# Kernel tuning notes

Hardware: AMD Instinct MI355X
Metric: run time of the kernel (lower is better)

## Reference

```python
import jax, jax.numpy as jnp
import numpy as np

GROUPS = 32
EPS = 1e-6


def group_norm(x, gamma, beta):
    b, c, h, w = x.shape
    xg = x.reshape(b, GROUPS, c // GROUPS, h, w)
    mean = xg.mean(axis=(2, 3, 4), keepdims=True)
    var = xg.var(axis=(2, 3, 4), keepdims=True)
    xn = (xg - mean) * jax.lax.rsqrt(var + EPS)
    xn = xn.reshape(b, c, h, w)
    return xn * gamma[None, :, None, None] + beta[None, :, None, None]


def conv1x1(x, w, b):
    # x: [B,C,H,W], w: [O,C], b: [O]
    return jnp.einsum('bchw,oc->bohw', x, w) + b[None, :, None, None]


def setup_inputs() -> dict:
    key = jax.random.key(0)
    ks = jax.random.split(key, 6)
    C = 512
    B, H, W = 2, 64, 64
    s = (C) ** -0.5  # fan-in style init scale for 1x1 convs
    return {
        'x': jax.random.normal(ks[0], (B, C, H, W), jnp.float32),
        'gn_gamma': jnp.ones((C,), jnp.float32),
        'gn_beta': jnp.zeros((C,), jnp.float32),
        'wq': jax.random.normal(ks[1], (C, C), jnp.float32) * s,
        'bq': jnp.zeros((C,), jnp.float32),
        'wk': jax.random.normal(ks[2], (C, C), jnp.float32) * s,
        'bk': jnp.zeros((C,), jnp.float32),
        'wv': jax.random.normal(ks[3], (C, C), jnp.float32) * s,
        'bv': jnp.zeros((C,), jnp.float32),
        'wo': jax.random.normal(ks[4], (C, C), jnp.float32) * s,
        'bo': jnp.zeros((C,), jnp.float32),
    }


def reference(x, gn_gamma, gn_beta, wq, bq, wk, bk, wv, bv, wo, bo):
    b, c, h, w = x.shape
    n = h * w
    h_ = group_norm(x, gn_gamma, gn_beta)
    q = conv1x1(h_, wq, bq).reshape(b, c, n)   # [B,C,N]
    k = conv1x1(h_, wk, bk).reshape(b, c, n)   # [B,C,N]
    v = conv1x1(h_, wv, bv).reshape(b, c, n)   # [B,C,N]
    scale = jnp.asarray(int(c) ** (-0.5), x.dtype)
    # scores[b, nq, nk] = sum_c q[b,c,nq] * k[b,c,nk]
    scores = jnp.einsum('bcn,bcm->bnm', q, k) * scale
    attn = jax.nn.softmax(scores, axis=2)      # softmax over keys
    # out[b,c,nq] = sum_m v[b,c,m] * attn[b,nq,m]
    out = jnp.einsum('bcm,bnm->bcn', v, attn).reshape(b, c, h, w)
    out = conv1x1(out, wo, bo)
    return x + out
```

## Files before the change

### kernel.cpp

```cpp
#include <hip/hip_runtime.h>

typedef unsigned short u16;
typedef __attribute__((ext_vector_type(8))) unsigned short ushort8;
typedef __attribute__((ext_vector_type(8))) short bf16x8;
typedef __attribute__((ext_vector_type(4))) float f32x4;

#define DEVINL __device__ __forceinline__

DEVINL float bf2f(u16 u){ union{unsigned i; float f;} v; v.i = ((unsigned)u) << 16; return v.f; }
DEVINL u16 f2bf(float f){
  unsigned x = __builtin_bit_cast(unsigned, f);
  x += 0x7fffu + ((x >> 16) & 1u);
  return (u16)(x >> 16);
}
DEVINL void gl_lds16(const void* g, void* l){
  __builtin_amdgcn_global_load_lds((const __attribute__((address_space(1))) unsigned*)g,
                                   (__attribute__((address_space(3))) unsigned*)l, 16, 0, 0);
}
template<int N> DEVINL void wait_vmcnt(){
  asm volatile("s_waitcnt vmcnt(%0)" :: "n"(N) : "memory");
}
DEVINL void hard_barrier(){
  asm volatile("" ::: "memory");
  __builtin_amdgcn_s_barrier();
  asm volatile("" ::: "memory");
}
DEVINL float wsum(float v){
  #pragma unroll
  for (int o = 32; o; o >>= 1) v += __shfl_xor(v, o, 64);
  return v;
}

__global__ __launch_bounds__(256) void prep_k(const float* __restrict__ s0, const float* __restrict__ s1,
                 const float* __restrict__ s2, const float* __restrict__ s3,
                 const float* __restrict__ bq, const float* __restrict__ bk, const float* __restrict__ bv,
                 const float* __restrict__ x,
                 u16* __restrict__ wdst, float* __restrict__ bdst, float* __restrict__ psum2){
  const int bx = blockIdx.x, t = threadIdx.x;
  if (bx < 512){
    const int g = bx >> 7;
    const float* src = (g==0) ? s0 : (g==1) ? s1 : (g==2) ? s2 : s3;
    const int i = ((bx & 127)*256 + t)*8;
    float4 f0 = *(const float4*)(src + i);
    float4 f1 = *(const float4*)(src + i + 4);
    ushort8 o;
    o[0]=f2bf(f0.x); o[1]=f2bf(f0.y); o[2]=f2bf(f0.z); o[3]=f2bf(f0.w);
    o[4]=f2bf(f1.x); o[5]=f2bf(f1.y); o[6]=f2bf(f1.z); o[7]=f2bf(f1.w);
    *(ushort8*)(wdst + g*262144 + i) = o;
    return;
  }
  if (bx == 512){
    for (int j = t; j < 1536; j += 256)
      bdst[j] = (j < 512) ? bq[j] : (j < 1024) ? bk[j-512] : bv[j-1024];
    return;
  }
  __shared__ __align__(16) float red[8];
  const int idx = bx - 513;
  const int grp = idx >> 2, chunk = idx & 3;
  const float* px = x + (size_t)grp*65536 + chunk*16384;
  float s = 0.f, ss = 0.f;
  for (int off = t*4; off < 16384; off += 1024){
    float4 u = *(const float4*)(px + off);
    s  += u.x + u.y + u.z + u.w;
    ss += u.x*u.x + u.y*u.y + u.z*u.z + u.w*u.w;
  }
  s = wsum(s); ss = wsum(ss);
  if ((t & 63) == 0){ red[t>>6] = s; red[4+(t>>6)] = ss; }
  __syncthreads();
  if (t == 0){
    psum2[(grp*4 + chunk)*2]     = red[0]+red[1]+red[2]+red[3];
    psum2[(grp*4 + chunk)*2 + 1] = red[4]+red[5]+red[6]+red[7];
  }
}

__global__ __launch_bounds__(256) void reduce4_k(const u16* __restrict__ part,
                 const float* __restrict__ psum, u16* __restrict__ dst){
  __shared__ float invsh[4];
  const int t = threadIdx.x, w = t>>6, ln = t&63;
  const int row = blockIdx.x*4 + w;
  float s = psum[ln*8192 + blockIdx.y*4096 + row];
  s = wsum(s);
  if (ln == 0) invsh[w] = 1.f / s;
  __syncthreads();
  const int i = (blockIdx.x*256 + t)*8;
  const u16* p = part + (size_t)blockIdx.y*8388608;
  float a[8] = {};
  #pragma unroll
  for (int ks = 0; ks < 4; ++ks){
    ushort8 u = *(const ushort8*)(p + (size_t)ks*2097152 + i);
    #pragma unroll
    for (int j = 0; j < 8; ++j) a[j] += bf2f(u[j]);
  }
  const float iv = invsh[w];
  ushort8 o;
  #pragma unroll
  for (int j = 0; j < 8; ++j) o[j] = f2bf(a[j] * iv);
  *(ushort8*)(dst + (size_t)blockIdx.y*2097152 + i) = o;
}

__global__ __launch_bounds__(256) void gn_apply_k(const float* __restrict__ x, const float* __restrict__ gamma,
                 const float* __restrict__ beta, const float* __restrict__ psum2, u16* __restrict__ ht){
  __shared__ __align__(16) u16 tile[32*512];
  __shared__ float gstat[64];
  const int b = blockIdx.y, n0 = blockIdx.x*32, t = threadIdx.x;
  if (t < 32){
    const float* pp = psum2 + ((b*32 + t)*4)*2;
    float S1 = pp[0]+pp[2]+pp[4]+pp[6];
    float S2 = pp[1]+pp[3]+pp[5]+pp[7];
    float mean = S1 * (1.f/65536.f);
    float var  = S2 * (1.f/65536.f) - mean*mean;
    gstat[t*2]   = mean;
    gstat[t*2+1] = rsqrtf(var + 1e-6f);
  }
  __syncthreads();
  #pragma unroll
  for (int it = 0; it < 8; ++it){
    int c  = it*64 + (t>>2);
    int nn = (t&3)*8;
    const float* px = x + ((size_t)(b*512 + c) << 12) + n0 + nn;
    float4 u0 = *(const float4*)(px);
    float4 u1 = *(const float4*)(px + 4);
    float mean = gstat[(c>>4)*2];
    float rstd = gstat[(c>>4)*2 + 1];
    float ga = gamma[c], be = beta[c];
    float f[8] = {u0.x,u0.y,u0.z,u0.w,u1.x,u1.y,u1.z,u1.w};
    #pragma unroll
    for (int j = 0; j < 8; ++j)
      tile[(nn+j)*512 + c] = f2bf((f[j] - mean) * rstd * ga + be);
  }
  __syncthreads();
  const int rw = t>>3, sg = t&7;
  #pragma unroll
  for (int uu = 0; uu < 8; ++uu){
    ushort8 v = *(const ushort8*)(tile + rw*512 + sg*64 + uu*8);
    *(ushort8*)(ht + ((size_t)(b*4096 + n0 + rw) << 9) + sg*64 + uu*8) = v;
  }
}

template<bool EXPSUM>
__global__ __launch_bounds__(512) void gemm8_nt(
    const u16* __restrict__ A, const u16* __restrict__ Bt, u16* __restrict__ C,
    float* __restrict__ psum,
    int K, int lda, int ldb, int ldc, int zdiv,
    long long aStrB, long long aStr, long long bStrB, long long bStr,
    long long cStrB, long long cStr)
{
  extern __shared__ __align__(16) char smem[];
  const int z = blockIdx.z, z1 = z / zdiv, z2 = z % zdiv;
  A  += (size_t)aStrB*z1 + (size_t)aStr*z2;
  Bt += (size_t)bStrB*z1 + (size_t)bStr*z2;
  C  += (size_t)cStrB*z1 + (size_t)cStr*z2;
  const int nwg = gridDim.x*gridDim.y;
  int wg = blockIdx.y*gridDim.x + blockIdx.x;
  wg = (wg & 7)*(nwg >> 3) + (wg >> 3);
  const int m0 = (wg / gridDim.x)*256, n0 = (wg % gridDim.x)*256;

  const int t = threadIdx.x, wv = t>>6, ln = t&63;
  const int wm = wv>>2, wn = wv&3;
  const int lq = ln&15, lg = ln>>4;
  const int srow = ln>>2;
  const int sseg = (((ln&3) ^ ((srow>>1)&3)))*8;
  const int rslot = (lg ^ ((lq>>1)&3))*16;

  auto STAGE_A = [&](int u){
    char* base = smem + (u&1)*16384 + wv*1024;
    const u16* g = A + (size_t)(m0 + wv*16 + srow)*lda + u*32 + sseg;
    gl_lds16(g, base);
    gl_lds16(g + (size_t)128*lda, base + 8192);
  };
  auto STAGE_B = [&](int u){
    char* base = smem + 32768 + (u&1)*16384 + wv*1024;
    const u16* g = Bt + (size_t)(n0 + wv*16 + srow)*ldb + u*32 + sseg;
    gl_lds16(g, base);
    gl_lds16(g + (size_t)128*ldb, base + 8192);
  };
  auto LDA4 = [&](int u, int mh, bf16x8* a){
    const char* p = smem + (u&1)*16384 + (wm*128 + mh*64 + lq)*64 + rslot;
    #pragma unroll
    for (int i = 0; i < 4; ++i) a[i] = *(const bf16x8*)(p + i*1024);
  };
  auto LDB4 = [&](int u, bf16x8* b){
    const char* p = smem + 32768 + (u&1)*16384 + (wn*64 + lq)*64 + rslot;
    #pragma unroll
    for (int j = 0; j < 4; ++j) b[j] = *(const bf16x8*)(p + j*1024);
  };

  f32x4 acc[8][4] = {};
  auto MFMA16 = [&](bf16x8* a4, bf16x8* b4, int moff){
    __builtin_amdgcn_s_setprio(1);
    #pragma unroll
    for (int n = 0; n < 4; ++n)
      #pragma unroll
      for (int m = 0; m < 4; ++m)
        acc[moff+m][n] = __builtin_amdgcn_mfma_f32_16x16x32_bf16(a4[m], b4[n], acc[moff+m][n], 0, 0, 0);
    __builtin_amdgcn_s_setprio(0);
  };

  STAGE_A(0); STAGE_B(0);
  const int U = K >> 5;
  for (int u = 0; u < U; ++u){
    wait_vmcnt<0>();
    hard_barrier();
    bf16x8 a0[4], a1[4], b[4];
    LDA4(u, 0, a0); LDB4(u, b);
    if (u + 1 < U){ STAGE_A(u+1); STAGE_B(u+1); }
    MFMA16(a0, b, 0);
    LDA4(u, 1, a1);
    MFMA16(a1, b, 4);
  }
  const int slice = EXPSUM ? ((n0 >> 8)*4 + wn) : 0;
  #pragma unroll
  for (int m = 0; m < 8; ++m)
    #pragma unroll
    for (int r2 = 0; r2 < 4; ++r2){
      const int mg = m0 + wm*128 + m*16 + lg*4 + r2;
      u16* cp = C + (size_t)mg*ldc + n0 + wn*64 + lq;
      if constexpr (EXPSUM){
        float e[4], rs = 0.f;
        #pragma unroll
        for (int n = 0; n < 4; ++n){ e[n] = __expf(acc[m][n][r2]); rs += e[n]; }
        rs += __shfl_xor(rs, 1, 64);
        rs += __shfl_xor(rs, 2, 64);
        rs += __shfl_xor(rs, 4, 64);
        rs += __shfl_xor(rs, 8, 64);
        if (lq == 0) psum[slice*8192 + z1*4096 + mg] = rs;
        #pragma unroll
        for (int n = 0; n < 4; ++n) cp[n*16] = f2bf(e[n]);
      } else {
        #pragma unroll
        for (int n = 0; n < 4; ++n) cp[n*16] = f2bf(acc[m][n][r2]);
      }
    }
}

__global__ __launch_bounds__(256) void qkv_k(
    const u16* __restrict__ Wstk, const u16* __restrict__ ht,
    const float* __restrict__ biases, u16* __restrict__ dstBase)
{
  __shared__ __align__(16) char smem[32768];
  char* smA0 = smem;
  char* smA1 = smem + 8192;
  char* smB0 = smem + 16384;
  char* smB1 = smem + 24576;
  const int z = blockIdx.z, mat = z >> 1, b = z & 1;
  const u16* A  = Wstk + mat*262144;
  const u16* Bt = ht + (size_t)b*2097152;
  const float* bias = biases + mat*512;
  const float oscale = (mat == 0) ? 0.044194173824159216f : 1.0f;
  u16* dst = dstBase + (size_t)mat*4194304 + (size_t)b*2097152;
  const int m0 = blockIdx.y*128, n0 = blockIdx.x*128;
  const int t = threadIdx.x, wv = t>>6, ln = t&63;
  const int wm = wv>>1, wn = wv&1;
  const int lq = ln&15, lg = ln>>4;
  const int srow = ln>>2;
  const int sseg = (((ln&3) ^ ((srow>>1)&3)))*8;
  const int rslot = (lg ^ ((lq>>1)&3))*16;
  f32x4 acc[4][4] = {};
  for (int kk = 0; kk < 512; kk += 64){
    __syncthreads();
    #pragma unroll
    for (int r = 0; r < 2; ++r){
      const int rr = r*64 + wv*16;
      const u16* pa = A  + (size_t)(m0 + rr + srow)*512 + kk + sseg;
      const u16* pb = Bt + (size_t)(n0 + rr + srow)*512 + kk + sseg;
      gl_lds16(pa,      smA0 + rr*64);
      gl_lds16(pa + 32, smA1 + rr*64);
      gl_lds16(pb,      smB0 + rr*64);
      gl_lds16(pb + 32, smB1 + rr*64);
    }
    __syncthreads();
    #pragma unroll
    for (int half = 0; half < 2; ++half){
      const char* pA = half ? smA1 : smA0;
      const char* pB = half ? smB1 : smB0;
      bf16x8 af[4], bfv[4];
      #pragma unroll
      for (int i = 0; i < 4; ++i) af[i]  = *(const bf16x8*)(pA + ((wm*64 + i*16 + lq)<<6) + rslot);
      #pragma unroll
      for (int j = 0; j < 4; ++j) bfv[j] = *(const bf16x8*)(pB + ((wn*64 + j*16 + lq)<<6) + rslot);
      #pragma unroll
      for (int i = 0; i < 4; ++i)
        #pragma unroll
        for (int j = 0; j < 4; ++j)
          acc[i][j] = __builtin_amdgcn_mfma_f32_16x16x32_bf16(af[i], bfv[j], acc[i][j], 0, 0, 0);
    }
  }
  if (mat == 2){
    #pragma unroll
    for (int i = 0; i < 4; ++i)
      #pragma unroll
      for (int r2 = 0; r2 < 4; ++r2){
        const int mg = m0 + wm*64 + i*16 + lg*4 + r2;
        float bv = bias[mg];
        #pragma unroll
        for (int j = 0; j < 4; ++j){
          const int ng = n0 + wn*64 + j*16 + lq;
          dst[(size_t)mg*4096 + ng] = f2bf(acc[i][j][r2] + bv);
        }
      }
  } else {
    __syncthreads();
    u16* ct = (u16*)smem;
    #pragma unroll
    for (int i = 0; i < 4; ++i)
      #pragma unroll
      for (int j = 0; j < 4; ++j)
        #pragma unroll
        for (int r2 = 0; r2 < 4; ++r2){
          const int ml = wm*64 + i*16 + lg*4 + r2;
          const int nl = wn*64 + j*16 + lq;
          ct[nl*128 + ml] = f2bf((acc[i][j][r2] + bias[m0 + ml]) * oscale);
        }
    __syncthreads();
    const int rw = t>>1, hf = (t&1)*64;
    #pragma unroll
    for (int u = 0; u < 8; ++u){
      *(ushort8*)(dst + (size_t)(n0 + rw)*512 + m0 + hf + u*8) =
          *(const ushort8*)(ct + rw*128 + hf + u*8);
    }
  }
}

template<bool TRANS_OUT, bool HAS_BIAS, bool HAS_RES, bool F32OUT>
__global__ __launch_bounds__(256) void gemm_nt(
    const u16* __restrict__ A, const u16* __restrict__ Bt,
    const float* __restrict__ bias, const float* __restrict__ res, void* __restrict__ Cw_,
    int K, int lda, int ldb, int ldc, int zdiv,
    long long aStrB, long long aStr, long long bStrB, long long bStr,
    long long cStrB, long long cStr, long long rStrB, float oscale)
{
  __shared__ __align__(16) char smem[32768];
  char* smA0 = smem;
  char* smA1 = smem + 8192;
  char* smB0 = smem + 16384;
  char* smB1 = smem + 24576;
  const int z = blockIdx.z;
  const int z1 = z / zdiv, z2 = z % zdiv;
  A  += (size_t)aStrB*z1 + (size_t)aStr*z2;
  Bt += (size_t)bStrB*z1 + (size_t)bStr*z2;
  u16*   Cw16 = (u16*)Cw_   + (size_t)cStrB*z1 + (size_t)cStr*z2;
  float* Cw32 = (float*)Cw_ + (size_t)cStrB*z1 + (size_t)cStr*z2;
  const float* resp = HAS_RES ? (res + (size_t)rStrB*z1) : nullptr;
  const int m0 = blockIdx.y*128, n0 = blockIdx.x*128;
  const int t = threadIdx.x, wv = t>>6, ln = t&63;
  const int wm = wv>>1, wn = wv&1;
  const int lq = ln&15, lg = ln>>4;
  const int srow = ln>>2;
  const int sseg = (((ln&3) ^ ((srow>>1)&3)))*8;
  const int rslot = (lg ^ ((lq>>1)&3))*16;
  f32x4 acc[4][4] = {};
  for (int kk = 0; kk < K; kk += 64){
    __syncthreads();
    #pragma unroll
    for (int r = 0; r < 2; ++r){
      const int rr = r*64 + wv*16;
      const u16* pa = A  + (size_t)(m0 + rr + srow)*lda + kk + sseg;
      const u16* pb = Bt + (size_t)(n0 + rr + srow)*ldb + kk + sseg;
      gl_lds16(pa,      smA0 + rr*64);
      gl_lds16(pa + 32, smA1 + rr*64);
      gl_lds16(pb,      smB0 + rr*64);
      gl_lds16(pb + 32, smB1 + rr*64);
    }
    __syncthreads();
    #pragma unroll
    for (int half = 0; half < 2; ++half){
      const char* pA = half ? smA1 : smA0;
      const char* pB = half ? smB1 : smB0;
      bf16x8 af[4], bfv[4];
      #pragma unroll
      for (int i = 0; i < 4; ++i) af[i]  = *(const bf16x8*)(pA + ((wm*64 + i*16 + lq)<<6) + rslot);
      #pragma unroll
      for (int j = 0; j < 4; ++j) bfv[j] = *(const bf16x8*)(pB + ((wn*64 + j*16 + lq)<<6) + rslot);
      #pragma unroll
      for (int i = 0; i < 4; ++i)
        #pragma unroll
        for (int j = 0; j < 4; ++j)
          acc[i][j] = __builtin_amdgcn_mfma_f32_16x16x32_bf16(af[i], bfv[j], acc[i][j], 0, 0, 0);
    }
  }
  if constexpr (!TRANS_OUT){
    #pragma unroll
    for (int i = 0; i < 4; ++i){
      #pragma unroll
      for (int r2 = 0; r2 < 4; ++r2){
        const int mg = m0 + wm*64 + i*16 + lg*4 + r2;
        float bv = HAS_BIAS ? bias[mg] : 0.f;
        #pragma unroll
        for (int j = 0; j < 4; ++j){
          const int ng = n0 + wn*64 + j*16 + lq;
          float v = (acc[i][j][r2] + bv) * oscale;
          if (HAS_RES) v += resp[(size_t)mg*ldc + ng];
          if constexpr (F32OUT) Cw32[(size_t)mg*ldc + ng] = v;
          else                  Cw16[(size_t)mg*ldc + ng] = f2bf(v);
        }
      }
    }
  } else {
    __syncthreads();
    u16* ct = (u16*)smem;
    #pragma unroll
    for (int i = 0; i < 4; ++i)
      #pragma unroll
      for (int j = 0; j < 4; ++j)
        #pragma unroll
        for (int r2 = 0; r2 < 4; ++r2){
          const int ml = wm*64 + i*16 + lg*4 + r2;
          const int nl = wn*64 + j*16 + lq;
          float v = acc[i][j][r2];
          if (HAS_BIAS) v += bias[m0 + ml];
          ct[nl*128 + ml] = f2bf(v * oscale);
        }
    __syncthreads();
    const int rw = t>>1, hf = (t&1)*64;
    #pragma unroll
    for (int u = 0; u < 8; ++u){
      *(ushort8*)(Cw16 + (size_t)(n0 + rw)*ldc + m0 + hf + u*8) =
          *(const ushort8*)(ct + rw*128 + hf + u*8);
    }
  }
}

extern "C" void kernel_launch(void* const* d_in, const int* in_sizes, int n_in,
                              void* d_out, int out_size, void* d_ws, size_t ws_size,
                              hipStream_t stream)
{
  const float* x   = (const float*)d_in[0];
  const float* gam = (const float*)d_in[1];
  const float* bet = (const float*)d_in[2];
  const float* wq  = (const float*)d_in[3];
  const float* bq  = (const float*)d_in[4];
  const float* wk  = (const float*)d_in[5];
  const float* bk  = (const float*)d_in[6];
  const float* wvp = (const float*)d_in[7];
  const float* bv  = (const float*)d_in[8];
  const float* wo  = (const float*)d_in[9];
  const float* bo  = (const float*)d_in[10];
  float* out = (float*)d_out;

  char* w = (char*)d_ws;
  float* psum2   = (float*)w;
  float* psum    = (float*)(w + 4096);
  float* biasQKV = (float*)(w + 2134016);
  u16* wqb  = (u16*)(w + (size_t)4194304);
  u16* wob  = wqb + 3*262144;
  u16* Qt   = wqb + 4*262144;
  u16* Kt   = Qt + 4194304;
  u16* Vb   = Kt + 4194304;
  u16* attT = Vb + 4194304;
  u16* Sbuf = attT + 4194304;
  u16* part = Sbuf + 33554432;
  u16* ht   = (u16*)d_out;

  const long long NC = 4096LL*512, NN = 4096LL*4096;

  prep_k<<<dim3(769), dim3(256), 0, stream>>>(wq, wk, wvp, wo, bq, bk, bv, x, wqb, biasQKV, psum2);
  gn_apply_k<<<dim3(128,2), dim3(256), 0, stream>>>(x, gam, bet, psum2, ht);
  qkv_k<<<dim3(32,4,6), dim3(256), 0, stream>>>(wqb, ht, biasQKV, Qt);
  gemm8_nt<true><<<dim3(16,16,2), dim3(512), 65536, stream>>>(
      Qt, Kt, Sbuf, psum, 512, 512, 512, 4096, 1, NC, 0, NC, 0, NN, 0);
  gemm8_nt<false><<<dim3(2,16,8), dim3(512), 65536, stream>>>(
      Sbuf, Vb, part, nullptr, 1024, 4096, 4096, 512, 4,
      NN, 1024, NC, 1024, 8388608, 2097152);
  reduce4_k<<<dim3(1024,2), dim3(256), 0, stream>>>(part, psum, attT);
  gemm_nt<false, true, true, true><<<dim3(32,4,2), dim3(256), 0, stream>>>(
      wob, attT, bo, x, out, 512, 512, 512, 4096, 1, 0,0, NC,0, NC,0, NC, 1.0f);
}
```

Before: 167.5 us.

## Fuse split-K reduction into output projection and move softmax normalization into PV epilogue

Removes the separate reduce4 kernel and the attT intermediate buffer. A tiny rowinv kernel computes the per-row 1/sum of the softmax denominators. The PV GEMM epilogue then scales its partial results by that value. The output projection kernel sums the four split-K partials while loading its B tile, replacing the async global-to-LDS load with register loads plus LDS stores. This saves one full write and read of the attention output, at the cost of a slower, non-async B operand load path in final_k.

```diff
diff --git a/kernel.cpp b/kernel.cpp
--- a/kernel.cpp
+++ b/kernel.cpp
@@ -73,29 +73,12 @@
   }
 }
 
-__global__ __launch_bounds__(256) void reduce4_k(const u16* __restrict__ part,
-                 const float* __restrict__ psum, u16* __restrict__ dst){
-  __shared__ float invsh[4];
-  const int t = threadIdx.x, w = t>>6, ln = t&63;
-  const int row = blockIdx.x*4 + w;
-  float s = psum[ln*8192 + blockIdx.y*4096 + row];
-  s = wsum(s);
-  if (ln == 0) invsh[w] = 1.f / s;
-  __syncthreads();
-  const int i = (blockIdx.x*256 + t)*8;
-  const u16* p = part + (size_t)blockIdx.y*8388608;
-  float a[8] = {};
-  #pragma unroll
-  for (int ks = 0; ks < 4; ++ks){
-    ushort8 u = *(const ushort8*)(p + (size_t)ks*2097152 + i);
-    #pragma unroll
-    for (int j = 0; j < 8; ++j) a[j] += bf2f(u[j]);
-  }
-  const float iv = invsh[w];
-  ushort8 o;
-  #pragma unroll
-  for (int j = 0; j < 8; ++j) o[j] = f2bf(a[j] * iv);
-  *(ushort8*)(dst + (size_t)blockIdx.y*2097152 + i) = o;
+__global__ __launch_bounds__(256) void rowinv_k(const float* __restrict__ psum, float* __restrict__ inv){
+  const int row = blockIdx.x*256 + threadIdx.x;
+  float s = 0.f;
+  #pragma unroll 8
+  for (int sl = 0; sl < 64; ++sl) s += psum[sl*8192 + row];
+  inv[row] = 1.f / s;
 }
 
 __global__ __launch_bounds__(256) void gn_apply_k(const float* __restrict__ x, const float* __restrict__ gamma,
@@ -137,10 +120,10 @@
   }
 }
 
-template<bool EXPSUM>
+template<bool EXPSUM, bool NORM>
 __global__ __launch_bounds__(512) void gemm8_nt(
     const u16* __restrict__ A, const u16* __restrict__ Bt, u16* __restrict__ C,
-    float* __restrict__ psum,
+    float* __restrict__ fp,
     int K, int lda, int ldb, int ldc, int zdiv,
     long long aStrB, long long aStr, long long bStrB, long long bStr,
     long long cStrB, long long cStr)
@@ -223,9 +206,13 @@
         rs += __shfl_xor(rs, 2, 64);
         rs += __shfl_xor(rs, 4, 64);
         rs += __shfl_xor(rs, 8, 64);
-        if (lq == 0) psum[slice*8192 + z1*4096 + mg] = rs;
+        if (lq == 0) fp[slice*8192 + z1*4096 + mg] = rs;
         #pragma unroll
         for (int n = 0; n < 4; ++n) cp[n*16] = f2bf(e[n]);
+      } else if constexpr (NORM){
+        const float iv = fp[z1*4096 + mg];
+        #pragma unroll
+        for (int n = 0; n < 4; ++n) cp[n*16] = f2bf(acc[m][n][r2] * iv);
       } else {
         #pragma unroll
         for (int n = 0; n < 4; ++n) cp[n*16] = f2bf(acc[m][n][r2]);
@@ -321,26 +308,19 @@
   }
 }
 
-template<bool TRANS_OUT, bool HAS_BIAS, bool HAS_RES, bool F32OUT>
-__global__ __launch_bounds__(256) void gemm_nt(
-    const u16* __restrict__ A, const u16* __restrict__ Bt,
-    const float* __restrict__ bias, const float* __restrict__ res, void* __restrict__ Cw_,
-    int K, int lda, int ldb, int ldc, int zdiv,
-    long long aStrB, long long aStr, long long bStrB, long long bStr,
-    long long cStrB, long long cStr, long long rStrB, float oscale)
+__global__ __launch_bounds__(256) void final_k(
+    const u16* __restrict__ Wo, const u16* __restrict__ part,
+    const float* __restrict__ bias, const float* __restrict__ x, float* __restrict__ out)
 {
   __shared__ __align__(16) char smem[32768];
   char* smA0 = smem;
   char* smA1 = smem + 8192;
   char* smB0 = smem + 16384;
   char* smB1 = smem + 24576;
-  const int z = blockIdx.z;
-  const int z1 = z / zdiv, z2 = z % zdiv;
-  A  += (size_t)aStrB*z1 + (size_t)aStr*z2;
-  Bt += (size_t)bStrB*z1 + (size_t)bStr*z2;
-  u16*   Cw16 = (u16*)Cw_   + (size_t)cStrB*z1 + (size_t)cStr*z2;
-  float* Cw32 = (float*)Cw_ + (size_t)cStrB*z1 + (size_t)cStr*z2;
-  const float* resp = HAS_RES ? (res + (size_t)rStrB*z1) : nullptr;
+  const int b = blockIdx.z;
+  const u16* pb4 = part + (size_t)b*8388608;
+  const float* resp = x + (size_t)b*2097152;
+  float* outp = out + (size_t)b*2097152;
   const int m0 = blockIdx.y*128, n0 = blockIdx.x*128;
   const int t = threadIdx.x, wv = t>>6, ln = t&63;
   const int wm = wv>>1, wn = wv&1;
@@ -349,17 +329,28 @@
   const int sseg = (((ln&3) ^ ((srow>>1)&3)))*8;
   const int rslot = (lg ^ ((lq>>1)&3))*16;
   f32x4 acc[4][4] = {};
-  for (int kk = 0; kk < K; kk += 64){
+  for (int kk = 0; kk < 512; kk += 64){
     __syncthreads();
     #pragma unroll
     for (int r = 0; r < 2; ++r){
       const int rr = r*64 + wv*16;
-      const u16* pa = A  + (size_t)(m0 + rr + srow)*lda + kk + sseg;
-      const u16* pb = Bt + (size_t)(n0 + rr + srow)*ldb + kk + sseg;
+      const u16* pa = Wo + (size_t)(m0 + rr + srow)*512 + kk + sseg;
       gl_lds16(pa,      smA0 + rr*64);
       gl_lds16(pa + 32, smA1 + rr*64);
-      gl_lds16(pb,      smB0 + rr*64);
-      gl_lds16(pb + 32, smB1 + rr*64);
+      const size_t boff = (size_t)(n0 + rr + srow)*512 + kk + sseg;
+      float s0[8] = {}, s1[8] = {};
+      #pragma unroll
+      for (int ks = 0; ks < 4; ++ks){
+        ushort8 u0 = *(const ushort8*)(pb4 + (size_t)ks*2097152 + boff);
+        ushort8 u1 = *(const ushort8*)(pb4 + (size_t)ks*2097152 + boff + 32);
+        #pragma unroll
+        for (int j = 0; j < 8; ++j){ s0[j] += bf2f(u0[j]); s1[j] += bf2f(u1[j]); }
+      }
+      ushort8 o0, o1;
+      #pragma unroll
+      for (int j = 0; j < 8; ++j){ o0[j] = f2bf(s0[j]); o1[j] = f2bf(s1[j]); }
+      *(ushort8*)(smB0 + rr*64 + ln*16) = o0;
+      *(ushort8*)(smB1 + rr*64 + ln*16) = o1;
     }
     __syncthreads();
     #pragma unroll
@@ -378,44 +369,17 @@
           acc[i][j] = __builtin_amdgcn_mfma_f32_16x16x32_bf16(af[i], bfv[j], acc[i][j], 0, 0, 0);
     }
   }
-  if constexpr (!TRANS_OUT){
-    #pragma unroll
-    for (int i = 0; i < 4; ++i){
-      #pragma unroll
-      for (int r2 = 0; r2 < 4; ++r2){
-        const int mg = m0 + wm*64 + i*16 + lg*4 + r2;
-        float bv = HAS_BIAS ? bias[mg] : 0.f;
-        #pragma unroll
-        for (int j = 0; j < 4; ++j){
-          const int ng = n0 + wn*64 + j*16 + lq;
-          float v = (acc[i][j][r2] + bv) * oscale;
-          if (HAS_RES) v += resp[(size_t)mg*ldc + ng];
-          if constexpr (F32OUT) Cw32[(size_t)mg*ldc + ng] = v;
-          else                  Cw16[(size_t)mg*ldc + ng] = f2bf(v);
-        }
+  #pragma unroll
+  for (int i = 0; i < 4; ++i){
+    #pragma unroll
+    for (int r2 = 0; r2 < 4; ++r2){
+      const int mg = m0 + wm*64 + i*16 + lg*4 + r2;
+      float bv = bias[mg];
+      #pragma unroll
+      for (int j = 0; j < 4; ++j){
+        const int ng = n0 + wn*64 + j*16 + lq;
+        outp[(size_t)mg*4096 + ng] = acc[i][j][r2] + bv + resp[(size_t)mg*4096 + ng];
       }
-    }
-  } else {
-    __syncthreads();
-    u16* ct = (u16*)smem;
-    #pragma unroll
-    for (int i = 0; i < 4; ++i)
-      #pragma unroll
-      for (int j = 0; j < 4; ++j)
-        #pragma unroll
-        for (int r2 = 0; r2 < 4; ++r2){
-          const int ml = wm*64 + i*16 + lg*4 + r2;
-          const int nl = wn*64 + j*16 + lq;
-          float v = acc[i][j][r2];
-          if (HAS_BIAS) v += bias[m0 + ml];
-          ct[nl*128 + ml] = f2bf(v * oscale);
-        }
-    __syncthreads();
-    const int rw = t>>1, hf = (t&1)*64;
-    #pragma unroll
-    for (int u = 0; u < 8; ++u){
-      *(ushort8*)(Cw16 + (size_t)(n0 + rw)*ldc + m0 + hf + u*8) =
-          *(const ushort8*)(ct + rw*128 + hf + u*8);
     }
   }
 }
@@ -440,14 +404,14 @@
   char* w = (char*)d_ws;
   float* psum2   = (float*)w;
   float* psum    = (float*)(w + 4096);
+  float* inv     = (float*)(w + 2101248);
   float* biasQKV = (float*)(w + 2134016);
   u16* wqb  = (u16*)(w + (size_t)4194304);
   u16* wob  = wqb + 3*262144;
   u16* Qt   = wqb + 4*262144;
   u16* Kt   = Qt + 4194304;
   u16* Vb   = Kt + 4194304;
-  u16* attT = Vb + 4194304;
-  u16* Sbuf = attT + 4194304;
+  u16* Sbuf = Vb + 4194304;
   u16* part = Sbuf + 33554432;
   u16* ht   = (u16*)d_out;
 
@@ -456,12 +420,11 @@
   prep_k<<<dim3(769), dim3(256), 0, stream>>>(wq, wk, wvp, wo, bq, bk, bv, x, wqb, biasQKV, psum2);
   gn_apply_k<<<dim3(128,2), dim3(256), 0, stream>>>(x, gam, bet, psum2, ht);
   qkv_k<<<dim3(32,4,6), dim3(256), 0, stream>>>(wqb, ht, biasQKV, Qt);
-  gemm8_nt<true><<<dim3(16,16,2), dim3(512), 65536, stream>>>(
+  gemm8_nt<true,false><<<dim3(16,16,2), dim3(512), 65536, stream>>>(
       Qt, Kt, Sbuf, psum, 512, 512, 512, 4096, 1, NC, 0, NC, 0, NN, 0);
-  gemm8_nt<false><<<dim3(2,16,8), dim3(512), 65536, stream>>>(
-      Sbuf, Vb, part, nullptr, 1024, 4096, 4096, 512, 4,
+  rowinv_k<<<dim3(32), dim3(256), 0, stream>>>(psum, inv);
+  gemm8_nt<false,true><<<dim3(2,16,8), dim3(512), 65536, stream>>>(
+      Sbuf, Vb, part, inv, 1024, 4096, 4096, 512, 4,
       NN, 1024, NC, 1024, 8388608, 2097152);
-  reduce4_k<<<dim3(1024,2), dim3(256), 0, stream>>>(part, psum, attT);
-  gemm_nt<false, true, true, true><<<dim3(32,4,2), dim3(256), 0, stream>>>(
-      wob, attT, bo, x, out, 512, 512, 512, 4096, 1, 0,0, NC,0, NC,0, NC, 1.0f);
-}
+  final_k<<<dim3(32,4,2), dim3(256), 0, stream>>>(wob, part, bo, x, out);
+}
```

Result: no change. 169.2 us (+1.0%).
